# Optimization experiments

Hardware: AMD Instinct MI355X
Metric: run time of the kernel (lower is better)

Reference implementation:

```python
import jax, jax.numpy as jnp
import numpy as np

Q = 2.0
TEMPERATURE = 1.0
EXP = 1.0 / (Q - 1.0)  # exponent 1/(q-1); q=2 -> sparsemax-style projection
N_BISECT_ITERS = 50    # enough for xtol ~ 1e-6 over an interval of width ~ (u_max - u_min + 10)


def setup_inputs() -> dict:
    key = jax.random.key(0)
    k_x, k_w1, k_w2 = jax.random.split(key, 3)
    B, D, H, E = 8192, 4096, 256, 64
    x = jax.random.normal(k_x, (B, D), dtype=jnp.float32)
    w1 = jax.random.normal(k_w1, (D, H), dtype=jnp.float32) * 0.02
    b1 = jnp.zeros((H,), dtype=jnp.float32)
    w2 = jax.random.normal(k_w2, (H, E), dtype=jnp.float32) * 0.05
    b2 = jnp.zeros((E,), dtype=jnp.float32)
    return {"x": x, "w1": w1, "b1": b1, "w2": w2, "b2": b2}


def _bisect_tau(us):
    # us: [B, E] = utilities / temperature. Find per-row tau with sum(relu(us - tau)**EXP) = 1.
    lo = jnp.min(us, axis=-1) - 10.0   # constraint(lo) > 0
    hi = jnp.max(us, axis=-1)          # constraint(hi) = -1 < 0

    def body(i, carry):
        lo, hi = carry
        mid = 0.5 * (lo + hi)
        f = jnp.sum(jnp.maximum(us - mid[..., None], 0.0) ** EXP, axis=-1) - 1.0
        pos = f > 0.0  # constraint is decreasing in tau: root is above mid
        return (jnp.where(pos, mid, lo), jnp.where(pos, hi, mid))

    lo, hi = jax.lax.fori_loop(0, N_BISECT_ITERS, body, (lo, hi))
    return 0.5 * (lo + hi)  # [B]


def reference(x, w1, b1, w2, b2):
    # utility_net (Dropout is identity in eval mode)
    h = jax.nn.relu(x @ w1 + b1)            # [B, 256]
    utilities = h @ w2 + b2                  # [B, E]
    us = utilities / TEMPERATURE
    # tau is found by root-finding on detached values in the original (.item()),
    # so it is a constant w.r.t. differentiation.
    tau = jax.lax.stop_gradient(_bisect_tau(jax.lax.stop_gradient(us)))
    p = jnp.maximum(us - tau[..., None], 0.0) ** EXP   # [B, E]
    p = p / (jnp.sum(p, axis=-1, keepdims=True) + 1e-8)
    return p
```

## Files before the change

### kernel.cpp

```cpp
#include <hip/hip_runtime.h>
#include <stdint.h>

typedef _Float16 f16;
typedef _Float16 f16x8 __attribute__((ext_vector_type(8)));
typedef float f32x4 __attribute__((ext_vector_type(4)));

#define D_DIM 4096
#define H_DIM 256
#define E_DIM 64
#define BM 128
#define KSPLIT 4
#define NKT2 16
#define HP_SLICE (8192 * 256)

__global__ void pack_kernel(const float* __restrict__ w1, f16* __restrict__ w1s,
                            const float* __restrict__ w2, f16* __restrict__ w2s) {
  const int b = blockIdx.x;
  const int t = threadIdx.x;
  if (b < 512) {
    const int u = b * 256 + t;
    const int lane = u & 63;
    const int kk = (u >> 6) & 1;
    const int c16 = (u >> 7) & 15;
    const int kt = u >> 11;
    const int g = lane >> 4, r = lane & 15;
    const int k0 = kt * 64 + kk * 32 + g * 8;
    const int col = c16 * 16 + r;
    f16x8 o;
#pragma unroll
    for (int j = 0; j < 8; ++j) o[j] = (f16)w1[(size_t)(k0 + j) * H_DIM + col];
    *(f16x8*)(w1s + (size_t)u * 8) = o;
  } else {
    const int u = (b - 512) * 256 + t;
    const int lane = u & 63;
    const int ks = (u >> 6) & 7;
    const int cg = u >> 9;
    const int g = lane >> 4, r = lane & 15;
    const int k0 = ks * 32 + g * 8;
    const int col = cg * 16 + r;
    f16x8 o;
#pragma unroll
    for (int j = 0; j < 8; ++j) o[j] = (f16)w2[(size_t)(k0 + j) * E_DIM + col];
    *(f16x8*)(w2s + (size_t)u * 8) = o;
  }
}

__launch_bounds__(512, 2)
__global__ void gemm1_splitk_kernel(const float* __restrict__ x,
                                    const f16* __restrict__ w1s,
                                    f16* __restrict__ hpart) {
  __shared__ __align__(16) float xbuf[4][BM * 64];

  const int t = threadIdx.x;
  const int lane = t & 63;
  const int wn = t >> 6;
  const int wm = wn >> 2, wc = wn & 3;
  const int g = lane >> 4, r = lane & 15;
  const int bid = blockIdx.x;
  const int ks = bid & 3;
  const int brow = (bid >> 2) * BM;
  const int kph = (bid * 5) & 15;
#define KT(s) ((kph + (s)) & 15)

  const int drow = lane >> 4;
  int hbo[4];
#pragma unroll
  for (int i = 0; i < 4; ++i) hbo[i] = ((lane & 15) ^ ((i * 4 + drow) & 15)) * 4;
  const float* dbase = x + (size_t)(brow + wn * 16 + drow) * D_DIM + ks * 1024;

  const f16* bptr = w1s + (size_t)ks * (16 * 16384) + (size_t)(wc * 8) * 512 + lane * 8;

  f32x4 acc[4][4];
#pragma unroll
  for (int mf = 0; mf < 4; ++mf)
#pragma unroll
    for (int nf = 0; nf < 4; ++nf) acc[mf][nf] = (f32x4){0.f, 0.f, 0.f, 0.f};

  f16x8 BE[8], BO[8];

#define GLDS(bufidx, kt)                                                        \
  {                                                                             \
    _Pragma("unroll") for (int i = 0; i < 4; ++i) {                             \
      const float* gp_ = dbase + (size_t)(i * 4) * D_DIM + (kt) * 64 + hbo[i];  \
      __builtin_amdgcn_global_load_lds(                                         \
          (const __attribute__((address_space(1))) void*)gp_,                   \
          (__attribute__((address_space(3))) void*)&xbuf[bufidx][(wn * 4 + i) * 256], \
          16, 0, 0);                                                            \
    }                                                                           \
  }
#define LDB(kt, B)                                                      \
  {                                                                     \
    const f16* p_ = bptr + (size_t)(kt) * 16384;                        \
    _Pragma("unroll") for (int q = 0; q < 8; ++q)                       \
      (B)[q] = *(const f16x8*)(p_ + q * 512);                           \
  }
#define COMP(bufidx, B)                                                         \
  {                                                                             \
    _Pragma("unroll") for (int kk = 0; kk < 2; ++kk) {                          \
      _Pragma("unroll") for (int mf = 0; mf < 4; ++mf) {                        \
        const int row_ = wm * 64 + mf * 16 + r;                                 \
        const float* bp_ = &xbuf[bufidx][row_ * 64];                            \
        const int L0_ = kk * 8 + g * 2;                                         \
        const float4 a0_ = *(const float4*)(bp_ + ((L0_ ^ r) << 2));            \
        const float4 a1_ = *(const float4*)(bp_ + (((L0_ + 1) ^ r) << 2));      \
        f16x8 af_;                                                              \
        af_[0] = (f16)a0_.x; af_[1] = (f16)a0_.y;                               \
        af_[2] = (f16)a0_.z; af_[3] = (f16)a0_.w;                               \
        af_[4] = (f16)a1_.x; af_[5] = (f16)a1_.y;                               \
        af_[6] = (f16)a1_.z; af_[7] = (f16)a1_.w;                               \
        _Pragma("unroll") for (int nf = 0; nf < 4; ++nf)                        \
          acc[mf][nf] = __builtin_amdgcn_mfma_f32_16x16x32_f16(                 \
              af_, (B)[nf * 2 + kk], acc[mf][nf], 0, 0, 0);                     \
      }                                                                         \
    }                                                                           \
  }
#define STEP(s, bidx, B)                                  \
  {                                                       \
    GLDS(((s) + 2) & 3, KT((s) + 2));                     \
    asm volatile("s_waitcnt vmcnt(16)" ::: "memory");     \
    __builtin_amdgcn_s_barrier();                         \
    COMP(bidx, B);                                        \
    LDB(KT((s) + 2), B);                                  \
  }
#define STEPN(s, bidx, B, WAIT)                           \
  {                                                       \
    asm volatile(WAIT ::: "memory");                      \
    __builtin_amdgcn_s_barrier();                         \
    COMP(bidx, B);                                        \
  }

  GLDS(0, KT(0));
  LDB(KT(0), BE);
  GLDS(1, KT(1));
  LDB(KT(1), BO);

#pragma unroll 1
  for (int q = 0; q < 3; ++q) {
    const int s0 = q * 4;
    STEP(s0 + 0, 0, BE);
    STEP(s0 + 1, 1, BO);
    STEP(s0 + 2, 2, BE);
    STEP(s0 + 3, 3, BO);
  }
  STEP(12, 0, BE);
  STEP(13, 1, BO);
  STEPN(14, 2, BE, "s_waitcnt vmcnt(12)");
  STEPN(15, 3, BO, "s_waitcnt vmcnt(0)");

  f16* hp = hpart + (size_t)ks * HP_SLICE + (size_t)brow * H_DIM;
#pragma unroll
  for (int mf = 0; mf < 4; ++mf)
#pragma unroll
    for (int nf = 0; nf < 4; ++nf) {
      const int col = wc * 64 + nf * 16 + r;
#pragma unroll
      for (int j = 0; j < 4; ++j) {
        const int row = wm * 64 + mf * 16 + g * 4 + j;
        hp[(size_t)row * H_DIM + col] = (f16)acc[mf][nf][j];
      }
    }
}

__launch_bounds__(512)
__global__ void reduce_fused_kernel(const f16* __restrict__ hpart,
                                    const float* __restrict__ b1,
                                    const f16* __restrict__ w2s,
                                    const float* __restrict__ b2,
                                    float* __restrict__ out) {
  __shared__ __align__(16) char smem[24576];
  f16* h_lds = (f16*)smem;
  float* u_lds = (float*)(smem + 16384);

  const int t = threadIdx.x;
  const int lane = t & 63;
  const int wn = t >> 6;
  const int g = lane >> 4, r = lane & 15;
  const int brow = blockIdx.x * 32;

  const int row = t >> 4;
  const int col0 = (t & 15) << 4;
  const f16* base = hpart + (size_t)(brow + row) * H_DIM + col0;
  float a[16];
#pragma unroll
  for (int j = 0; j < 16; ++j) a[j] = 0.f;
#pragma unroll
  for (int c = 0; c < KSPLIT; ++c) {
    const f16x8 va = *(const f16x8*)(base + (size_t)c * HP_SLICE);
    const f16x8 vb = *(const f16x8*)(base + (size_t)c * HP_SLICE + 8);
#pragma unroll
    for (int j = 0; j < 8; ++j) { a[j] += (float)va[j]; a[8 + j] += (float)vb[j]; }
  }
  {
    const int s8 = (row & 7) << 3;
    f16x8 h0, h1;
#pragma unroll
    for (int j = 0; j < 8; ++j) {
      h0[j] = (f16)fmaxf(a[j] + b1[col0 + j], 0.f);
      h1[j] = (f16)fmaxf(a[8 + j] + b1[col0 + 8 + j], 0.f);
    }
    *(f16x8*)(h_lds + row * 256 + (col0 ^ s8)) = h0;
    *(f16x8*)(h_lds + row * 256 + ((col0 + 8) ^ s8)) = h1;
  }
  __syncthreads();

  const int rh2 = wn & 1;
  const int cg = wn >> 1;
  f32x4 acc2 = {0.f, 0.f, 0.f, 0.f};
  const f16* w2p = w2s + (size_t)(cg * 8) * 512 + lane * 8;
#pragma unroll
  for (int ksi = 0; ksi < 8; ++ksi) {
    const int arow = rh2 * 16 + r;
    const int kb = ksi * 32 + g * 8;
    const f16x8 af = *(const f16x8*)(h_lds + arow * 256 + (kb ^ ((arow & 7) << 3)));
    const f16x8 bf = *(const f16x8*)(w2p + ksi * 512);
    acc2 = __builtin_amdgcn_mfma_f32_16x16x32_f16(af, bf, acc2, 0, 0, 0);
  }
  {
    const int col = cg * 16 + r;
    const float bias = b2[col];
#pragma unroll
    for (int j = 0; j < 4; ++j) {
      const int rr = rh2 * 16 + g * 4 + j;
      u_lds[rr * 64 + col] = acc2[j] + bias;
    }
  }
  __syncthreads();

  const int srow = wn * 4 + (lane >> 4);
  const int scol = (lane & 15) << 2;
  const float4 uv = *(const float4*)(u_lds + srow * 64 + scol);
  float u0 = uv.x, u1 = uv.y, u2 = uv.z, u3 = uv.w;

  float mx = fmaxf(fmaxf(u0, u1), fmaxf(u2, u3));
  float mn = fminf(fminf(u0, u1), fminf(u2, u3));
#pragma unroll
  for (int m = 1; m < 16; m <<= 1) {
    mx = fmaxf(mx, __shfl_xor(mx, m));
    mn = fminf(mn, __shfl_xor(mn, m));
  }
  float lo = mn - 10.0f, hi = mx;
#pragma unroll 1
  for (int it = 0; it < 32; ++it) {
    const float mid = 0.5f * (lo + hi);
    float sm = fmaxf(u0 - mid, 0.f) + fmaxf(u1 - mid, 0.f) +
               fmaxf(u2 - mid, 0.f) + fmaxf(u3 - mid, 0.f);
#pragma unroll
    for (int m = 1; m < 16; m <<= 1) sm += __shfl_xor(sm, m);
    const bool pos = (sm - 1.0f) > 0.0f;
    lo = pos ? mid : lo;
    hi = pos ? hi : mid;
  }
  const float tau = 0.5f * (lo + hi);
  const float p0 = fmaxf(u0 - tau, 0.f);
  const float p1 = fmaxf(u1 - tau, 0.f);
  const float p2 = fmaxf(u2 - tau, 0.f);
  const float p3 = fmaxf(u3 - tau, 0.f);
  float sum = p0 + p1 + p2 + p3;
#pragma unroll
  for (int m = 1; m < 16; m <<= 1) sum += __shfl_xor(sum, m);
  const float inv = 1.0f / (sum + 1e-8f);
  float4 pv;
  pv.x = p0 * inv; pv.y = p1 * inv; pv.z = p2 * inv; pv.w = p3 * inv;
  *(float4*)(out + (size_t)(brow + srow) * E_DIM + scol) = pv;
}

extern "C" void kernel_launch(void* const* d_in, const int* in_sizes, int n_in,
                              void* d_out, int out_size, void* d_ws, size_t ws_size,
                              hipStream_t stream) {
  const float* x  = (const float*)d_in[0];
  const float* w1 = (const float*)d_in[1];
  const float* b1 = (const float*)d_in[2];
  const float* w2 = (const float*)d_in[3];
  const float* b2 = (const float*)d_in[4];
  float* out = (float*)d_out;

  char* wsb = (char*)d_ws;
  f16* w1s = (f16*)wsb;
  f16* w2s = (f16*)(wsb + (2u << 20));
  f16* hpart = (f16*)(wsb + (4u << 20));

  pack_kernel<<<520, 256, 0, stream>>>(w1, w1s, w2, w2s);
  gemm1_splitk_kernel<<<256, 512, 0, stream>>>(x, w1s, hpart);
  reduce_fused_kernel<<<256, 512, 0, stream>>>(hpart, b1, w2s, b2, out);
}
```

Measured before the change: 53.07 us.

## Halve GEMM1 LDS staging to double-buffering to fit more blocks per CU

```diff
diff --git a/kernel.cpp b/kernel.cpp
--- a/kernel.cpp
+++ b/kernel.cpp
@@ -3,6 +3,7 @@
 
 typedef _Float16 f16;
 typedef _Float16 f16x8 __attribute__((ext_vector_type(8)));
+typedef _Float16 f16x4 __attribute__((ext_vector_type(4)));
 typedef float f32x4 __attribute__((ext_vector_type(4)));
 
 #define D_DIM 4096
@@ -45,11 +46,11 @@
   }
 }
 
-__launch_bounds__(512, 2)
+__launch_bounds__(512, 4)
 __global__ void gemm1_splitk_kernel(const float* __restrict__ x,
                                     const f16* __restrict__ w1s,
                                     f16* __restrict__ hpart) {
-  __shared__ __align__(16) float xbuf[4][BM * 64];
+  __shared__ __align__(16) float xbuf[2][BM * 64];
 
   const int t = threadIdx.x;
   const int lane = t & 63;
@@ -67,7 +68,6 @@
 #pragma unroll
   for (int i = 0; i < 4; ++i) hbo[i] = ((lane & 15) ^ ((i * 4 + drow) & 15)) * 4;
   const float* dbase = x + (size_t)(brow + wn * 16 + drow) * D_DIM + ks * 1024;
-
   const f16* bptr = w1s + (size_t)ks * (16 * 16384) + (size_t)(wc * 8) * 512 + lane * 8;
 
   f32x4 acc[4][4];
@@ -75,7 +75,6 @@
   for (int mf = 0; mf < 4; ++mf)
 #pragma unroll
     for (int nf = 0; nf < 4; ++nf) acc[mf][nf] = (f32x4){0.f, 0.f, 0.f, 0.f};
-
   f16x8 BE[8], BO[8];
 
 #define GLDS(bufidx, kt)                                                        \
@@ -84,7 +83,8 @@
       const float* gp_ = dbase + (size_t)(i * 4) * D_DIM + (kt) * 64 + hbo[i];  \
       __builtin_amdgcn_global_load_lds(                                         \
           (const __attribute__((address_space(1))) void*)gp_,                   \
-          (__attribute__((address_space(3))) void*)&xbuf[bufidx][(wn * 4 + i) * 256], \
+          (__attribute__((address_space(3))) void*)                             \
+              (&xbuf[bufidx][(wn * 4 + i) * 256]),                              \
           16, 0, 0);                                                            \
     }                                                                           \
   }
@@ -114,38 +114,24 @@
       }                                                                         \
     }                                                                           \
   }
-#define STEP(s, bidx, B)                                  \
+#define STEP(s, Bc, Bn)                                   \
   {                                                       \
-    GLDS(((s) + 2) & 3, KT((s) + 2));                     \
-    asm volatile("s_waitcnt vmcnt(16)" ::: "memory");     \
+    asm volatile("s_waitcnt vmcnt(8)" ::: "memory");      \
     __builtin_amdgcn_s_barrier();                         \
-    COMP(bidx, B);                                        \
-    LDB(KT((s) + 2), B);                                  \
-  }
-#define STEPN(s, bidx, B, WAIT)                           \
-  {                                                       \
-    asm volatile(WAIT ::: "memory");                      \
-    __builtin_amdgcn_s_barrier();                         \
-    COMP(bidx, B);                                        \
+    if ((s) + 1 < NKT2) GLDS(((s) + 1) & 1, KT((s) + 1)); \
+    COMP((s) & 1, Bc);                                    \
+    if ((s) + 1 < NKT2) LDB(KT((s) + 1), Bn);             \
   }
 
   GLDS(0, KT(0));
   LDB(KT(0), BE);
-  GLDS(1, KT(1));
-  LDB(KT(1), BO);
 
 #pragma unroll 1
-  for (int q = 0; q < 3; ++q) {
-    const int s0 = q * 4;
-    STEP(s0 + 0, 0, BE);
-    STEP(s0 + 1, 1, BO);
-    STEP(s0 + 2, 2, BE);
-    STEP(s0 + 3, 3, BO);
-  }
-  STEP(12, 0, BE);
-  STEP(13, 1, BO);
-  STEPN(14, 2, BE, "s_waitcnt vmcnt(12)");
-  STEPN(15, 3, BO, "s_waitcnt vmcnt(0)");
+  for (int q = 0; q < 8; ++q) {
+    const int s0 = q * 2;
+    STEP(s0 + 0, BE, BO);
+    STEP(s0 + 1, BO, BE);
+  }
 
   f16* hp = hpart + (size_t)ks * HP_SLICE + (size_t)brow * H_DIM;
 #pragma unroll
```

Result: slower. 107.3 us (+102.1%).
